# Kernel tuning notes

Measured on AMD Instinct MI355X. Metric: run time of the kernel, lower is better.

## Reference

```python
import jax, jax.numpy as jnp
import numpy as np

N_DOMAIN = 8
EPS = 1e-05
NUM_FEATURES = 1024
BATCH = 65536


def setup_inputs() -> dict:
    key = jax.random.key(0)
    k1, k2 = jax.random.split(key)
    x = jax.random.normal(k1, (BATCH, NUM_FEATURES), dtype=jnp.float32)
    y = jax.random.randint(k2, (BATCH,), 0, N_DOMAIN, dtype=jnp.int64)
    gamma = jnp.ones((1, NUM_FEATURES), dtype=jnp.float32)
    beta = jnp.zeros((1, NUM_FEATURES), dtype=jnp.float32)
    return {"x": x, "y": y, "gamma": gamma, "beta": beta}


def reference(x, y, gamma, beta):
    # Training-mode domain-specific batchnorm (2D path of DSBatchNorm2).
    y32 = y.astype(jnp.int32)
    ones = jnp.ones((x.shape[0],), dtype=x.dtype)
    count = jax.ops.segment_sum(ones, y32, num_segments=N_DOMAIN)  # [D]
    safe_count = jnp.maximum(count, 1.0)[:, None]                  # [D,1]
    # per-domain mean (biased var, two-pass to match ((x-mean)**2).mean)
    mean = jax.ops.segment_sum(x, y32, num_segments=N_DOMAIN) / safe_count  # [D,F]
    diff = x - mean[y32]                                                    # [N,F]
    var = jax.ops.segment_sum(diff * diff, y32, num_segments=N_DOMAIN) / safe_count
    x_hat = diff / jnp.sqrt(var[y32] + EPS)
    x_norm = gamma * x_hat + beta
    cnt_row = count[y32][:, None]  # [N,1]
    # count>1 -> normalized; count==1 -> raw x; count==0 unreachable
    out = jnp.where(cnt_row > 1.0, x_norm, jnp.where(cnt_row == 1.0, x, 0.0))
    return out
```

## Files before the change

### kernel.cpp

```cpp
#include <hip/hip_runtime.h>


#define NROW  65536
#define NFEAT 1024
#define NF4   256
#define NDOM  8
#define EPSV  1e-5f

#define WS_SUM   0
#define WS_SQ    8192
#define WS_CNT   16384
#define WS_OFFS  16392
#define WS_CUR   16401
#define WS_RIDX  16416
#define WS_SCL   49184
#define WS_BIA   57376
#define WS_ZERO_BYTES ((16384 + 8) * 4)

__global__ __launch_bounds__(256) void dsbn_hist(
    const int* __restrict__ y, unsigned* __restrict__ gcnt)
{
  __shared__ unsigned lh[NDOM];
  const int tid = threadIdx.x;
  if (tid < NDOM) lh[tid] = 0u;
  __syncthreads();
  const int r = blockIdx.x * 256 + tid;
  const int d = y[r] & 7;
  atomicAdd(&lh[d], 1u);
  __syncthreads();
  if (tid < NDOM) atomicAdd(&gcnt[tid], lh[tid]);
}

__global__ void dsbn_scan(const unsigned* __restrict__ gcnt,
                          unsigned* __restrict__ offs,
                          unsigned* __restrict__ cursor)
{
  if (threadIdx.x == 0) {
    unsigned c = 0;
    for (int d = 0; d < NDOM; ++d) { offs[d] = c; cursor[d] = c; c += gcnt[d]; }
    offs[NDOM] = c;
  }
}

__global__ __launch_bounds__(256) void dsbn_scatter(
    const int* __restrict__ y, unsigned* __restrict__ cursor,
    unsigned short* __restrict__ ridx)
{
  __shared__ unsigned lh[NDOM], lbase[NDOM];
  const int tid = threadIdx.x;
  if (tid < NDOM) lh[tid] = 0u;
  __syncthreads();
  const int r = blockIdx.x * 256 + tid;
  const int d = y[r] & 7;
  const unsigned rank = atomicAdd(&lh[d], 1u);
  __syncthreads();
  if (tid < NDOM) lbase[tid] = atomicAdd(&cursor[tid], lh[tid]);
  __syncthreads();
  ridx[lbase[d] + rank] = (unsigned short)r;
}

__global__ __launch_bounds__(256) void dsbn_stats(
    const float* __restrict__ x, const unsigned short* __restrict__ ridx,
    const unsigned* __restrict__ offs,
    float* __restrict__ gsum, float* __restrict__ gsq)
{
  const int tid   = threadIdx.x;
  const int w     = tid >> 6, lane = tid & 63;
  const int gw    = blockIdx.x * 4 + w;
  const int chunk = gw >> 2;
  const int ftile = gw & 3;
  const int c4    = ftile * 64 + lane;
  const int p0    = chunk * 32;

  const int myr = (int)ridx[p0 + (lane & 31)];

  int d0 = 0;
#pragma unroll
  for (int k = 1; k < NDOM; ++k) d0 += (p0 >= (int)offs[k]) ? 1 : 0;
  const bool single = (p0 + 32 <= (int)offs[d0 + 1]);

  const float4* __restrict__ x4 = reinterpret_cast<const float4*>(x);
  float4 s = make_float4(0.f, 0.f, 0.f, 0.f);
  float4 q = make_float4(0.f, 0.f, 0.f, 0.f);

  auto flush = [&](int dd) {
    float* gs = gsum + dd * NFEAT + c4 * 4;
    float* gq = gsq  + dd * NFEAT + c4 * 4;
    atomicAdd(gs + 0, s.x); atomicAdd(gs + 1, s.y);
    atomicAdd(gs + 2, s.z); atomicAdd(gs + 3, s.w);
    atomicAdd(gq + 0, q.x); atomicAdd(gq + 1, q.y);
    atomicAdd(gq + 2, q.z); atomicAdd(gq + 3, q.w);
  };

  if (single) {
#pragma unroll 4
    for (int k = 0; k < 32; ++k) {
      const int r = (int)__builtin_amdgcn_readlane((unsigned)myr, (unsigned)k);
      const float4 v = x4[(size_t)r * NF4 + c4];
      s.x += v.x; s.y += v.y; s.z += v.z; s.w += v.w;
      q.x = fmaf(v.x, v.x, q.x); q.y = fmaf(v.y, v.y, q.y);
      q.z = fmaf(v.z, v.z, q.z); q.w = fmaf(v.w, v.w, q.w);
    }
    flush(d0);
  } else {
    int d = d0;
    for (int k = 0; k < 32; ++k) {
      const int p = p0 + k;
      const int r = (int)__builtin_amdgcn_readlane((unsigned)myr, (unsigned)k);
      while (p >= (int)offs[d + 1]) {
        flush(d);
        s = make_float4(0.f, 0.f, 0.f, 0.f);
        q = make_float4(0.f, 0.f, 0.f, 0.f);
        ++d;
      }
      const float4 v = x4[(size_t)r * NF4 + c4];
      s.x += v.x; s.y += v.y; s.z += v.z; s.w += v.w;
      q.x = fmaf(v.x, v.x, q.x); q.y = fmaf(v.y, v.y, q.y);
      q.z = fmaf(v.z, v.z, q.z); q.w = fmaf(v.w, v.w, q.w);
    }
    flush(d);
  }
}

__global__ __launch_bounds__(256) void dsbn_prep(
    const float* __restrict__ gsum, const float* __restrict__ gsq,
    const unsigned* __restrict__ gcnt,
    const float* __restrict__ gamma, const float* __restrict__ beta,
    float* __restrict__ scl, float* __restrict__ bia)
{
  const int i = blockIdx.x * 256 + threadIdx.x;
  const int d = i >> 10;
  const int f = i & 1023;
  const float c    = (float)gcnt[d];
  const float sc   = fmaxf(c, 1.f);
  const float mean = gsum[i] / sc;
  float var = gsq[i] / sc - mean * mean;
  var = fmaxf(var, 0.f);
  float scale, bias;
  if (c > 1.5f) {
    const float inv = 1.f / sqrtf(var + EPSV);
    scale = gamma[f] * inv;
    bias  = fmaf(-mean, scale, beta[f]);
  } else if (c > 0.5f) {
    scale = 1.f; bias = 0.f;
  } else {
    scale = 0.f; bias = 0.f;
  }
  scl[i] = scale;
  bia[i] = bias;
}

__global__ __launch_bounds__(256) void dsbn_norm(
    const float* __restrict__ x, const unsigned short* __restrict__ ridx,
    const unsigned* __restrict__ offs,
    const float* __restrict__ scl, const float* __restrict__ bia,
    float* __restrict__ out)
{
  const int tid   = threadIdx.x;
  const int w     = tid >> 6, lane = tid & 63;
  const int gw    = blockIdx.x * 4 + w;
  const int chunk = gw >> 2;
  const int ftile = gw & 3;
  const int c4    = ftile * 64 + lane;
  const int p0    = chunk * 32;

  const int myr = (int)ridx[p0 + (lane & 31)];

  int d0 = 0;
#pragma unroll
  for (int k = 1; k < NDOM; ++k) d0 += (p0 >= (int)offs[k]) ? 1 : 0;
  const bool single = (p0 + 32 <= (int)offs[d0 + 1]);

  const float4* __restrict__ x4 = reinterpret_cast<const float4*>(x);
  const float4* __restrict__ s4 = reinterpret_cast<const float4*>(scl);
  const float4* __restrict__ b4 = reinterpret_cast<const float4*>(bia);
  float4* __restrict__ o4 = reinterpret_cast<float4*>(out);

  if (single) {
    const float4 sc = s4[d0 * NF4 + c4];
    const float4 bb = b4[d0 * NF4 + c4];
#pragma unroll 4
    for (int k = 0; k < 32; ++k) {
      const int r = (int)__builtin_amdgcn_readlane((unsigned)myr, (unsigned)k);
      const float4 v = x4[(size_t)r * NF4 + c4];
      float4 o;
      o.x = fmaf(v.x, sc.x, bb.x);
      o.y = fmaf(v.y, sc.y, bb.y);
      o.z = fmaf(v.z, sc.z, bb.z);
      o.w = fmaf(v.w, sc.w, bb.w);
      o4[(size_t)r * NF4 + c4] = o;
    }
  } else {
    int d = d0;
    for (int k = 0; k < 32; ++k) {
      const int p = p0 + k;
      const int r = (int)__builtin_amdgcn_readlane((unsigned)myr, (unsigned)k);
      while (p >= (int)offs[d + 1]) ++d;
      const float4 sc = s4[d * NF4 + c4];
      const float4 bb = b4[d * NF4 + c4];
      const float4 v = x4[(size_t)r * NF4 + c4];
      float4 o;
      o.x = fmaf(v.x, sc.x, bb.x);
      o.y = fmaf(v.y, sc.y, bb.y);
      o.z = fmaf(v.z, sc.z, bb.z);
      o.w = fmaf(v.w, sc.w, bb.w);
      o4[(size_t)r * NF4 + c4] = o;
    }
  }
}

extern "C" void kernel_launch(void* const* d_in, const int* in_sizes, int n_in,
                              void* d_out, int out_size, void* d_ws, size_t ws_size,
                              hipStream_t stream) {
  const float* x     = (const float*)d_in[0];
  const int*   y     = (const int*)  d_in[1];
  const float* gamma = (const float*)d_in[2];
  const float* beta  = (const float*)d_in[3];
  float* out = (float*)d_out;

  float*          ws     = (float*)d_ws;
  float*          gsum   = ws + WS_SUM;
  float*          gsq    = ws + WS_SQ;
  unsigned*       gcnt   = (unsigned*)(ws + WS_CNT);
  unsigned*       offs   = (unsigned*)(ws + WS_OFFS);
  unsigned*       cursor = (unsigned*)(ws + WS_CUR);
  unsigned short* ridx   = (unsigned short*)(ws + WS_RIDX);
  float*          scl    = ws + WS_SCL;
  float*          bia    = ws + WS_BIA;

  hipMemsetAsync(ws, 0, WS_ZERO_BYTES, stream);

  dsbn_hist   <<<dim3(256),  dim3(256), 0, stream>>>(y, gcnt);
  dsbn_scan   <<<dim3(1),    dim3(64),  0, stream>>>(gcnt, offs, cursor);
  dsbn_scatter<<<dim3(256),  dim3(256), 0, stream>>>(y, cursor, ridx);
  dsbn_stats  <<<dim3(2048), dim3(256), 0, stream>>>(x, ridx, offs, gsum, gsq);
  dsbn_prep   <<<dim3(32),   dim3(256), 0, stream>>>(gsum, gsq, gcnt, gamma, beta, scl, bia);
  dsbn_norm   <<<dim3(2048), dim3(256), 0, stream>>>(x, ridx, offs, scl, bia, out);
}
```

Before: 618.7 us.

## Replace global float atomics in stats with per-block partials and reduce kernel

The stats kernel now gives each block a 256-row group and a 64-float4 feature tile, each wave handling 64 rows. Single-domain blocks reduce their four waves through shared-memory atomics and write one partial sum/sumsq vector plus a domain tag to a workspace buffer. A new small reduce kernel, four blocks of 256 threads, accumulates tagged partials per domain in shared memory and adds them into the global sums. Boundary blocks still use global atomics. The aim is to remove most global float atomic traffic at the cost of an extra launch, a serial reduce over 256 partials per feature tile, and halved grid parallelism.

```diff
diff --git a/kernel.cpp b/kernel.cpp
--- a/kernel.cpp
+++ b/kernel.cpp
@@ -12,9 +12,10 @@
 #define WS_CNT   16384
 #define WS_OFFS  16392
 #define WS_CUR   16401
-#define WS_RIDX  16416
-#define WS_SCL   49184
-#define WS_BIA   57376
+#define WS_TAG   16412
+#define WS_RIDX  17440
+#define WS_PBUF  50208
+#define WS_SCL   574496
 #define WS_ZERO_BYTES ((16384 + 8) * 4)
 
 __global__ __launch_bounds__(256) void dsbn_hist(
@@ -62,50 +63,75 @@
 __global__ __launch_bounds__(256) void dsbn_stats(
     const float* __restrict__ x, const unsigned short* __restrict__ ridx,
     const unsigned* __restrict__ offs,
-    float* __restrict__ gsum, float* __restrict__ gsq)
-{
-  const int tid   = threadIdx.x;
-  const int w     = tid >> 6, lane = tid & 63;
-  const int gw    = blockIdx.x * 4 + w;
-  const int chunk = gw >> 2;
-  const int ftile = gw & 3;
-  const int c4    = ftile * 64 + lane;
-  const int p0    = chunk * 32;
-
-  const int myr = (int)ridx[p0 + (lane & 31)];
-
-  int d0 = 0;
+    float* __restrict__ gsum, float* __restrict__ gsq,
+    float4* __restrict__ pbuf, unsigned* __restrict__ tag)
+{
+  __shared__ float ls[NFEAT / 4];
+  __shared__ float lq[NFEAT / 4];
+
+  const int tid  = threadIdx.x;
+  const int w    = tid >> 6, lane = tid & 63;
+  const int ft   = blockIdx.x >> 8;
+  const int pg   = blockIdx.x & 255;
+  const int c4   = ft * 64 + lane;
+  const int p0w  = pg * 256 + w * 64;
+  const int pb0  = pg * 256;
+
+  ls[tid] = 0.f;
+  lq[tid] = 0.f;
+
+  int db = 0;
 #pragma unroll
-  for (int k = 1; k < NDOM; ++k) d0 += (p0 >= (int)offs[k]) ? 1 : 0;
-  const bool single = (p0 + 32 <= (int)offs[d0 + 1]);
-
+  for (int k = 1; k < NDOM; ++k) db += (pb0 >= (int)offs[k]) ? 1 : 0;
+  const bool bsingle = (pb0 + 256 <= (int)offs[db + 1]);
+
+  const int myr = (int)ridx[p0w + lane];
   const float4* __restrict__ x4 = reinterpret_cast<const float4*>(x);
+
   float4 s = make_float4(0.f, 0.f, 0.f, 0.f);
   float4 q = make_float4(0.f, 0.f, 0.f, 0.f);
 
-  auto flush = [&](int dd) {
-    float* gs = gsum + dd * NFEAT + c4 * 4;
-    float* gq = gsq  + dd * NFEAT + c4 * 4;
-    atomicAdd(gs + 0, s.x); atomicAdd(gs + 1, s.y);
-    atomicAdd(gs + 2, s.z); atomicAdd(gs + 3, s.w);
-    atomicAdd(gq + 0, q.x); atomicAdd(gq + 1, q.y);
-    atomicAdd(gq + 2, q.z); atomicAdd(gq + 3, q.w);
-  };
-
-  if (single) {
-#pragma unroll 4
-    for (int k = 0; k < 32; ++k) {
+  __syncthreads();
+
+  if (bsingle) {
+#pragma unroll 8
+    for (int k = 0; k < 64; ++k) {
       const int r = (int)__builtin_amdgcn_readlane((unsigned)myr, (unsigned)k);
       const float4 v = x4[(size_t)r * NF4 + c4];
       s.x += v.x; s.y += v.y; s.z += v.z; s.w += v.w;
       q.x = fmaf(v.x, v.x, q.x); q.y = fmaf(v.y, v.y, q.y);
       q.z = fmaf(v.z, v.z, q.z); q.w = fmaf(v.w, v.w, q.w);
     }
-    flush(d0);
+    const int j0 = lane * 4;
+    atomicAdd(&ls[j0 + 0], s.x); atomicAdd(&ls[j0 + 1], s.y);
+    atomicAdd(&ls[j0 + 2], s.z); atomicAdd(&ls[j0 + 3], s.w);
+    atomicAdd(&lq[j0 + 0], q.x); atomicAdd(&lq[j0 + 1], q.y);
+    atomicAdd(&lq[j0 + 2], q.z); atomicAdd(&lq[j0 + 3], q.w);
+    __syncthreads();
+    float4* pb = pbuf + (size_t)blockIdx.x * 128;
+    if (tid < 64) {
+      pb[tid] = make_float4(ls[tid * 4], ls[tid * 4 + 1],
+                            ls[tid * 4 + 2], ls[tid * 4 + 3]);
+    } else if (tid < 128) {
+      const int t = tid - 64;
+      pb[64 + t] = make_float4(lq[t * 4], lq[t * 4 + 1],
+                               lq[t * 4 + 2], lq[t * 4 + 3]);
+    }
+    if (tid == 0) tag[blockIdx.x] = (unsigned)db;
   } else {
-    int d = d0;
-    for (int k = 0; k < 32; ++k) {
-      const int p = p0 + k;
+    auto flush = [&](int dd) {
+      float* gs = gsum + dd * NFEAT + c4 * 4;
+      float* gq = gsq  + dd * NFEAT + c4 * 4;
+      atomicAdd(gs + 0, s.x); atomicAdd(gs + 1, s.y);
+      atomicAdd(gs + 2, s.z); atomicAdd(gs + 3, s.w);
+      atomicAdd(gq + 0, q.x); atomicAdd(gq + 1, q.y);
+      atomicAdd(gq + 2, q.z); atomicAdd(gq + 3, q.w);
+    };
+    int d = 0;
+#pragma unroll
+    for (int k = 1; k < NDOM; ++k) d += (p0w >= (int)offs[k]) ? 1 : 0;
+    for (int k = 0; k < 64; ++k) {
+      const int p = p0w + k;
       const int r = (int)__builtin_amdgcn_readlane((unsigned)myr, (unsigned)k);
       while (p >= (int)offs[d + 1]) {
         flush(d);
@@ -119,6 +145,47 @@
       q.z = fmaf(v.z, v.z, q.z); q.w = fmaf(v.w, v.w, q.w);
     }
     flush(d);
+    if (tid == 0) tag[blockIdx.x] = 0xFFFFFFFFu;
+  }
+}
+
+__global__ __launch_bounds__(256) void dsbn_reduce(
+    const float4* __restrict__ pbuf, const unsigned* __restrict__ tag,
+    float* __restrict__ gsum, float* __restrict__ gsq)
+{
+  __shared__ float lsum[NDOM][256];
+  __shared__ float lsq [NDOM][256];
+  const int tid = threadIdx.x;
+  const int w = tid >> 6, lane = tid & 63;
+  const int ft = blockIdx.x;
+
+  for (int i = tid; i < NDOM * 256; i += 256) {
+    (&lsum[0][0])[i] = 0.f;
+    (&lsq [0][0])[i] = 0.f;
+  }
+  __syncthreads();
+
+#pragma unroll 4
+  for (int gi = 0; gi < 64; ++gi) {
+    const int b = ft * 256 + w * 64 + gi;
+    const unsigned t = tag[b];
+    if (t > 7u) continue;
+    const float4 vs = pbuf[(size_t)b * 128 + lane];
+    const float4 vq = pbuf[(size_t)b * 128 + 64 + lane];
+    const int j0 = lane * 4;
+    atomicAdd(&lsum[t][j0 + 0], vs.x); atomicAdd(&lsum[t][j0 + 1], vs.y);
+    atomicAdd(&lsum[t][j0 + 2], vs.z); atomicAdd(&lsum[t][j0 + 3], vs.w);
+    atomicAdd(&lsq [t][j0 + 0], vq.x); atomicAdd(&lsq [t][j0 + 1], vq.y);
+    atomicAdd(&lsq [t][j0 + 2], vq.z); atomicAdd(&lsq [t][j0 + 3], vq.w);
+  }
+  __syncthreads();
+
+  for (int i = tid; i < NDOM * 256; i += 256) {
+    const int d = i >> 8;
+    const int f = i & 255;
+    const int cell = d * NFEAT + ft * 256 + f;
+    gsum[cell] += lsum[d][f];
+    gsq [cell] += lsq [d][f];
   }
 }
 
@@ -224,16 +291,19 @@
   unsigned*       gcnt   = (unsigned*)(ws + WS_CNT);
   unsigned*       offs   = (unsigned*)(ws + WS_OFFS);
   unsigned*       cursor = (unsigned*)(ws + WS_CUR);
+  unsigned*       tag    = (unsigned*)(ws + WS_TAG);
   unsigned short* ridx   = (unsigned short*)(ws + WS_RIDX);
-  float*          scl    = ws + WS_SCL;
-  float*          bia    = ws + WS_BIA;
+  float4*         pbuf   = (float4*)(ws + WS_PBUF);
+  float*          scl    = ws + WS_PBUF + 1024 * 128 * 4;
+  float*          bia    = scl + 8192;
 
   hipMemsetAsync(ws, 0, WS_ZERO_BYTES, stream);
 
   dsbn_hist   <<<dim3(256),  dim3(256), 0, stream>>>(y, gcnt);
   dsbn_scan   <<<dim3(1),    dim3(64),  0, stream>>>(gcnt, offs, cursor);
   dsbn_scatter<<<dim3(256),  dim3(256), 0, stream>>>(y, cursor, ridx);
-  dsbn_stats  <<<dim3(2048), dim3(256), 0, stream>>>(x, ridx, offs, gsum, gsq);
+  dsbn_stats  <<<dim3(1024), dim3(256), 0, stream>>>(x, ridx, offs, gsum, gsq, pbuf, tag);
+  dsbn_reduce <<<dim3(4),    dim3(256), 0, stream>>>(pbuf, tag, gsum, gsq);
   dsbn_prep   <<<dim3(32),   dim3(256), 0, stream>>>(gsum, gsq, gcnt, gamma, beta, scl, bia);
   dsbn_norm   <<<dim3(2048), dim3(256), 0, stream>>>(x, ridx, offs, scl, bia, out);
 }
```

New measurement: 720.2 us. +16.4%, slower.
